# Kernel optimization log

Measured on AMD Instinct MI355X. Metric: run time of the kernel, lower is better.

Reference implementation:

```python
import jax, jax.numpy as jnp
import numpy as np
from jax import lax

H, W = 14, 14          # spatial input_size
K = 6                  # mask_size (square)
ST = 2                 # mask_stride
_xs = np.arange(0, H - K + 1, ST)   # mask/window positions; (H-K)%ST==0 so grid matches avg_pool2d
M = len(_xs)
# pairwise rectangle-intersection coordinates between mask R1 (index a) and window W2 (index b)
_lo = np.maximum(_xs[:, None], _xs[None, :])                       # [M,M]
_hi = np.maximum(np.minimum(_xs[:, None] + K, _xs[None, :] + K), _lo)  # [M,M], clamped (empty -> zero area)


def setup_inputs() -> dict:
    key = jax.random.key(0)
    x = jax.random.normal(key, (32, 1000, H, W), dtype=jnp.float32)
    return {"x": x}


def _forward(x):
    B, C = x.shape[0], x.shape[1]
    total = jnp.sum(x, axis=(2, 3))  # [B,C]  == unmasked_logits
    # window sums == avg_pool2d(divisor_override=1); also equals sum over each mask region R1
    winsum = lax.reduce_window(x, 0.0, lax.add, (1, 1, K, K), (1, 1, ST, ST), 'VALID')  # [B,C,M,M]
    one_mask_logits = total[:, :, None, None] - winsum                # [B,C,M,M]
    one_mask_pred = jnp.argmax(one_mask_logits, axis=1)               # [B,M,M]
    pred = jnp.argmax(total, axis=1)                                  # [B]
    disagree = one_mask_pred != pred[:, None, None]                   # [B,M,M]

    # summed-area table for O(1) rectangle sums (zero-padded)
    sat = jnp.pad(jnp.cumsum(jnp.cumsum(x, axis=2), axis=3), ((0, 0), (0, 0), (1, 0), (1, 0)))
    xhi = _hi[:, None, :, None]; xlo = _lo[:, None, :, None]          # depend on (i, k)
    yhi = _hi[None, :, None, :]; ylo = _lo[None, :, None, :]          # depend on (j, l)
    # sum of x over R1(i,j) ∩ W2(k,l): [B,C,M,M,M,M]
    overlap = (sat[:, :, xhi, yhi] - sat[:, :, xlo, yhi]
               - sat[:, :, xhi, ylo] + sat[:, :, xlo, ylo])

    # two-mask logits: total - sum(R1) - sum(W2) + sum(R1 ∩ W2)
    two = (total[:, :, None, None, None, None]
           - winsum[:, :, :, :, None, None]
           - winsum[:, :, None, None, :, :]
           + overlap)                                                 # [B,C,M,M,M,M]
    two_pred = jnp.argmax(two, axis=1)                                # [B,M,M,M,M]

    # a disagreer (i,j) is confirmed if ALL second-mask preds equal its one-mask pred
    agree = jnp.all(two_pred == one_mask_pred[:, :, :, None, None], axis=(3, 4))  # [B,M,M]
    cand = (disagree & agree).reshape(B, -1)                          # row-major (i,j) order
    first = jnp.argmax(cand, axis=1)                                  # first confirmed disagreer
    new_pred = jnp.take_along_axis(one_mask_pred.reshape(B, -1), first[:, None], axis=1)[:, 0]
    pred = jnp.where(jnp.any(cand, axis=1), new_pred, pred)
    return pred, one_mask_logits


def reference(x):
    pred, _ = _forward(x)
    return pred
```

## Files before the change

kernel.cpp:

```cpp
#include <hip/hip_runtime.h>


#define NC 1000
#define NBC 32000
#define NCH 16
#define PSTRIDE 384

__host__ __device__ constexpr int tri_off(int p) { return p * 25 - p * (p - 1) / 2; }

__global__ __launch_bounds__(256) void satA(const float* __restrict__ x,
                                            float* __restrict__ Sws) {
    __shared__ float lx[64 * 197];
    const int tid = threadIdx.x;
    const int blk = blockIdx.x;
    const float4* x4 = reinterpret_cast<const float4*>(x) + (size_t)blk * 3136;
#pragma unroll
    for (int it = 0; it < 13; ++it) {
        int f = it * 256 + tid;
        if (f < 3136) {
            float4 v = x4[f];
            int img = f / 49;
            int off = f - img * 49;
            float* d = &lx[img * 197 + off * 4];
            d[0] = v.x; d[1] = v.y; d[2] = v.z; d[3] = v.w;
        }
    }
    __syncthreads();
    if (tid < 64) {
        const float* im = &lx[tid * 197];
        float S[8][8];
#pragma unroll
        for (int c = 0; c < 8; ++c) S[0][c] = 0.f;
        float colacc[7];
#pragma unroll
        for (int c = 0; c < 7; ++c) colacc[c] = 0.f;
#pragma unroll
        for (int r = 0; r < 7; ++r) {
            float rowf[28];
#pragma unroll
            for (int j = 0; j < 28; ++j) rowf[j] = im[r * 28 + j];
            S[r + 1][0] = 0.f;
            float run = 0.f;
#pragma unroll
            for (int c = 0; c < 7; ++c) {
                float blk2 = rowf[2 * c] + rowf[2 * c + 1] + rowf[14 + 2 * c] + rowf[14 + 2 * c + 1];
                colacc[c] += blk2;
                run += colacc[c];
                S[r + 1][c + 1] = run;
            }
        }
        const int bc = blk * 64 + tid;
#pragma unroll
        for (int k = 0; k < 64; ++k)
            Sws[(size_t)k * NBC + bc] = S[k >> 3][k & 7];
    }
}

__global__ __launch_bounds__(512) void kernB(const float* __restrict__ Sws,
                                             unsigned long long* __restrict__ part) {
    __shared__ float Sc[64][65];
    __shared__ float W[64][27];
    const int tid = threadIdx.x;
    const int b = blockIdx.x >> 4;
    const int wc = blockIdx.x & 15;
    const int c0 = (wc == 15) ? 936 : wc * 64;
    const int cl = tid & 63;
    const int hi = tid >> 6;

#pragma unroll
    for (int it = 0; it < 8; ++it) {
        const int k = it * 8 + hi;
        Sc[cl][k] = Sws[(size_t)k * NBC + b * NC + c0 + cl];
    }
    __syncthreads();

#pragma unroll
    for (int j = hi; j < 27; j += 8) {
        float v;
        if (j < 25) {
            const int p1 = j / 5, p2 = j % 5;
            v = ((Sc[cl][(p1 + 3) * 8 + p2 + 3] - Sc[cl][p1 * 8 + p2 + 3])
                 - Sc[cl][(p1 + 3) * 8 + p2]) + Sc[cl][p1 * 8 + p2];
        } else if (j == 25) {
            v = Sc[cl][63];
        } else {
            v = 0.f;
        }
        W[cl][j] = v;
    }
    __syncthreads();

    const int sid = tid;
    if (sid < 351) {
        int pi, qi, i0, i1, i2, i3;
        if (sid < 325) {
            int p = 0;
            while (tri_off(p + 1) <= sid) ++p;
            const int q = p + (sid - tri_off(p));
            const int p1 = p / 5, p2 = p % 5, q1 = q / 5, q2 = q % 5;
            const int rlo = (p1 > q1 ? p1 : q1);
            const int rmn = (p1 < q1 ? p1 : q1);
            const int rhi = (rmn + 3 > rlo ? rmn + 3 : rlo);
            const int clo = (p2 > q2 ? p2 : q2);
            const int cmn = (p2 < q2 ? p2 : q2);
            const int chi = (cmn + 3 > clo ? cmn + 3 : clo);
            pi = p; qi = q;
            i0 = rhi * 8 + chi; i1 = rlo * 8 + chi;
            i2 = rhi * 8 + clo; i3 = rlo * 8 + clo;
        } else if (sid < 350) {
            pi = sid - 325; qi = 26;
            i0 = i1 = i2 = i3 = 0;
        } else {
            pi = 26; qi = 26; i0 = i1 = i2 = i3 = 0;
        }
        float bv = -3.4e38f;
        int bc = 0;
#pragma unroll 4
        for (int c = 0; c < 64; ++c) {
            const float rect = ((Sc[c][i0] - Sc[c][i1]) - Sc[c][i2]) + Sc[c][i3];
            const float v = ((W[c][25] - W[c][pi]) - W[c][qi]) + rect;
            if (v > bv) { bv = v; bc = c; }
        }
        const unsigned u = __float_as_uint(bv);
        const unsigned fk = u ^ (unsigned)(((int)u >> 31) | 0x80000000);
        part[(size_t)(b * NCH + wc) * PSTRIDE + sid] =
            ((unsigned long long)fk << 32) | (unsigned)~(unsigned)(c0 + bc);
    }
}

__global__ __launch_bounds__(128) void kernC(const unsigned long long* __restrict__ part,
                                             int* __restrict__ out) {
    __shared__ unsigned long long mg[352];
    const int b = blockIdx.x;
    const int t = threadIdx.x;
    for (int s = t; s < 351; s += 128) {
        unsigned long long m = 0ull;
#pragma unroll
        for (int wc = 0; wc < NCH; ++wc) {
            unsigned long long v = part[(size_t)(b * NCH + wc) * PSTRIDE + s];
            if (v > m) m = v;
        }
        mg[s] = m;
    }
    __syncthreads();
    if (t < 64) {
        const unsigned predidx = (unsigned)mg[350];
        const int pred = (int)~predidx;
        bool cand = false;
        int p1 = 0;
        if (t < 25) {
            const unsigned p1i = (unsigned)mg[325 + t];
            p1 = (int)~p1i;
            bool ag = true;
            for (int j = 0; j < 25; ++j) {
                const int a = t < j ? t : j;
                const int q = t < j ? j : t;
                ag = ag && ((unsigned)mg[tri_off(a) + (q - a)] == p1i);
            }
            cand = ag && (p1 != pred);
        }
        const unsigned long long mask = __ballot(cand);
        int ans = pred;
        if (mask) ans = __shfl(p1, __ffsll(mask) - 1, 64);
        if (t == 0) out[b] = ans;
    }
}

extern "C" void kernel_launch(void* const* d_in, const int* in_sizes, int n_in,
                              void* d_out, int out_size, void* d_ws, size_t ws_size,
                              hipStream_t stream) {
    const float* x = (const float*)d_in[0];
    int* out = (int*)d_out;

    float* Sws = (float*)d_ws;
    unsigned long long* part =
        (unsigned long long*)((char*)d_ws + (size_t)64 * NBC * 4);

    satA<<<NBC / 64, 256, 0, stream>>>(x, Sws);
    kernB<<<32 * NCH, 512, 0, stream>>>(Sws, part);
    kernC<<<32, 128, 0, stream>>>(part, out);
}
```

Baseline: 84.23 us.

## Fuse summed-area-table construction into the argmax kernel via shared memory

Removes the separate satA kernel. Each kernB block now loads its own 64 channel images from x into shared memory and builds the 8x8 coarse SAT in place, overwriting the image rows. The window sums and pairwise argmax then read from that buffer. This drops the global write and re-read of the SAT workspace and one kernel launch. In exchange, each block runs a serial SAT phase on only 64 threads, and the block size shrinks to 384.

```diff
diff --git a/kernel.cpp b/kernel.cpp
--- a/kernel.cpp
+++ b/kernel.cpp
@@ -2,63 +2,14 @@
 
 
 #define NC 1000
-#define NBC 32000
 #define NCH 16
 #define PSTRIDE 384
 
 __host__ __device__ constexpr int tri_off(int p) { return p * 25 - p * (p - 1) / 2; }
 
-__global__ __launch_bounds__(256) void satA(const float* __restrict__ x,
-                                            float* __restrict__ Sws) {
+__global__ __launch_bounds__(384) void kernB(const float* __restrict__ x,
+                                             unsigned long long* __restrict__ part) {
     __shared__ float lx[64 * 197];
-    const int tid = threadIdx.x;
-    const int blk = blockIdx.x;
-    const float4* x4 = reinterpret_cast<const float4*>(x) + (size_t)blk * 3136;
-#pragma unroll
-    for (int it = 0; it < 13; ++it) {
-        int f = it * 256 + tid;
-        if (f < 3136) {
-            float4 v = x4[f];
-            int img = f / 49;
-            int off = f - img * 49;
-            float* d = &lx[img * 197 + off * 4];
-            d[0] = v.x; d[1] = v.y; d[2] = v.z; d[3] = v.w;
-        }
-    }
-    __syncthreads();
-    if (tid < 64) {
-        const float* im = &lx[tid * 197];
-        float S[8][8];
-#pragma unroll
-        for (int c = 0; c < 8; ++c) S[0][c] = 0.f;
-        float colacc[7];
-#pragma unroll
-        for (int c = 0; c < 7; ++c) colacc[c] = 0.f;
-#pragma unroll
-        for (int r = 0; r < 7; ++r) {
-            float rowf[28];
-#pragma unroll
-            for (int j = 0; j < 28; ++j) rowf[j] = im[r * 28 + j];
-            S[r + 1][0] = 0.f;
-            float run = 0.f;
-#pragma unroll
-            for (int c = 0; c < 7; ++c) {
-                float blk2 = rowf[2 * c] + rowf[2 * c + 1] + rowf[14 + 2 * c] + rowf[14 + 2 * c + 1];
-                colacc[c] += blk2;
-                run += colacc[c];
-                S[r + 1][c + 1] = run;
-            }
-        }
-        const int bc = blk * 64 + tid;
-#pragma unroll
-        for (int k = 0; k < 64; ++k)
-            Sws[(size_t)k * NBC + bc] = S[k >> 3][k & 7];
-    }
-}
-
-__global__ __launch_bounds__(512) void kernB(const float* __restrict__ Sws,
-                                             unsigned long long* __restrict__ part) {
-    __shared__ float Sc[64][65];
     __shared__ float W[64][27];
     const int tid = threadIdx.x;
     const int b = blockIdx.x >> 4;
@@ -67,22 +18,59 @@
     const int cl = tid & 63;
     const int hi = tid >> 6;
 
+    const float4* x4 = reinterpret_cast<const float4*>(x)
+                       + (size_t)(b * NC + c0) * 49;
 #pragma unroll
-    for (int it = 0; it < 8; ++it) {
-        const int k = it * 8 + hi;
-        Sc[cl][k] = Sws[(size_t)k * NBC + b * NC + c0 + cl];
+    for (int it = 0; it < 9; ++it) {
+        const int f = it * 384 + tid;
+        if (f < 3136) {
+            float4 v = x4[f];
+            const int img = f / 49;
+            const int off = f - img * 49;
+            float* d = &lx[img * 197 + off * 4];
+            d[0] = v.x; d[1] = v.y; d[2] = v.z; d[3] = v.w;
+        }
     }
     __syncthreads();
 
+    if (tid < 64) {
+        float* row = &lx[tid * 197];
+        float colacc[7];
 #pragma unroll
-    for (int j = hi; j < 27; j += 8) {
+        for (int c = 0; c < 7; ++c) colacc[c] = 0.f;
+#pragma unroll
+        for (int r = 0; r < 7; ++r) {
+            float rowf[28];
+#pragma unroll
+            for (int j = 0; j < 28; ++j) rowf[j] = row[r * 28 + j];
+            if (r == 0) {
+#pragma unroll
+                for (int j = 0; j < 8; ++j) row[j] = 0.f;
+            }
+            row[(r + 1) * 8] = 0.f;
+            float run = 0.f;
+#pragma unroll
+            for (int c = 0; c < 7; ++c) {
+                const float blk2 = rowf[2 * c] + rowf[2 * c + 1]
+                                 + rowf[14 + 2 * c] + rowf[14 + 2 * c + 1];
+                colacc[c] += blk2;
+                run += colacc[c];
+                row[(r + 1) * 8 + c + 1] = run;
+            }
+        }
+    }
+    __syncthreads();
+
+#define SC(c, k) lx[(c) * 197 + (k)]
+#pragma unroll
+    for (int j = hi; j < 27; j += 6) {
         float v;
         if (j < 25) {
             const int p1 = j / 5, p2 = j % 5;
-            v = ((Sc[cl][(p1 + 3) * 8 + p2 + 3] - Sc[cl][p1 * 8 + p2 + 3])
-                 - Sc[cl][(p1 + 3) * 8 + p2]) + Sc[cl][p1 * 8 + p2];
+            v = ((SC(cl, (p1 + 3) * 8 + p2 + 3) - SC(cl, p1 * 8 + p2 + 3))
+                 - SC(cl, (p1 + 3) * 8 + p2)) + SC(cl, p1 * 8 + p2);
         } else if (j == 25) {
-            v = Sc[cl][63];
+            v = SC(cl, 63);
         } else {
             v = 0.f;
         }
@@ -117,7 +105,7 @@
         int bc = 0;
 #pragma unroll 4
         for (int c = 0; c < 64; ++c) {
-            const float rect = ((Sc[c][i0] - Sc[c][i1]) - Sc[c][i2]) + Sc[c][i3];
+            const float rect = ((SC(c, i0) - SC(c, i1)) - SC(c, i2)) + SC(c, i3);
             const float v = ((W[c][25] - W[c][pi]) - W[c][qi]) + rect;
             if (v > bv) { bv = v; bc = c; }
         }
@@ -126,6 +114,7 @@
         part[(size_t)(b * NCH + wc) * PSTRIDE + sid] =
             ((unsigned long long)fk << 32) | (unsigned)~(unsigned)(c0 + bc);
     }
+#undef SC
 }
 
 __global__ __launch_bounds__(128) void kernC(const unsigned long long* __restrict__ part,
@@ -172,11 +161,8 @@
     const float* x = (const float*)d_in[0];
     int* out = (int*)d_out;
 
-    float* Sws = (float*)d_ws;
-    unsigned long long* part =
-        (unsigned long long*)((char*)d_ws + (size_t)64 * NBC * 4);
+    unsigned long long* part = (unsigned long long*)d_ws;
 
-    satA<<<NBC / 64, 256, 0, stream>>>(x, Sws);
-    kernB<<<32 * NCH, 512, 0, stream>>>(Sws, part);
+    kernB<<<32 * NCH, 384, 0, stream>>>(x, part);
     kernC<<<32, 128, 0, stream>>>(part, out);
 }
```

Measured after the change: 83.03 us. About the same (-1.4%).
